# Kernel optimization log

Hardware: AMD Instinct MI355X
Metric: run time of the kernel (lower is better)

Reference implementation:

```python
import jax, jax.numpy as jnp
import numpy as np

B, N, E, FIN, D, A = 64, 512, 2048, 300, 256, 64
NH = 4
EPS = 1e-5


def setup_inputs() -> dict:
    ks = jax.random.split(jax.random.key(0), 32)
    lengths = 256 + jax.random.randint(ks[0], (B,), 0, N - 256 + 1)
    L = lengths[:, None]
    r = jax.random.randint(ks[1], (B, E), 0, 1 << 30)
    c = jax.random.randint(ks[2], (B, E), 0, 1 << 30)
    edge_row = r % L                                   # src in [0, len)
    edge_col = (edge_row + 1 + c % (L - 1)) % L        # dst != src, in [0, len)
    w = lambda k, sh, fan: jax.random.normal(k, sh, jnp.float32) / np.float32(np.sqrt(fan))
    b = lambda k, sh: 0.01 * jax.random.normal(k, sh, jnp.float32)
    return dict(
        x=jax.random.normal(ks[3], (B, N, FIN), jnp.float32),
        edge_attr=jax.random.normal(ks[4], (B, E, A), jnp.float32),
        edge_row=edge_row, edge_col=edge_col, lengths=lengths,
        W1=w(ks[5], (D, FIN), FIN), W2=w(ks[6], (D, A), A),
        W3=w(ks[7], (D, 2 * D), 2 * D), b3=b(ks[8], (D,)), gcn_bias=b(ks[9], (D,)),
        bn1_g=jnp.ones((D,)), bn1_b=jnp.zeros((D,)),
        in_proj_w=w(ks[10], (3 * D, D), D), in_proj_b=b(ks[11], (3 * D,)),
        out_proj_w=w(ks[12], (D, D), D), out_proj_b=b(ks[13], (D,)),
        ln1_g=jnp.ones((D,)), ln1_b=jnp.zeros((D,)),
        lin1_w=w(ks[14], (4 * D, D), D), lin1_b=b(ks[15], (4 * D,)),
        lin2_w=w(ks[16], (D, 4 * D), 4 * D), lin2_b=b(ks[17], (D,)),
        ln2_g=jnp.ones((D,)), ln2_b=jnp.zeros((D,)),
        bn2_g=jnp.ones((D,)), bn2_b=jnp.zeros((D,)),
        lin_w=w(ks[18], (2, 2 * D), 2 * D), lin_b=b(ks[19], (2,)),
        bn3_g=jnp.ones((2,)), bn3_b=jnp.zeros((2,)),
    )


def _bn(x, g, bt, axes):
    m = jnp.mean(x, axes, keepdims=True)
    v = jnp.mean((x - m) ** 2, axes, keepdims=True)
    return (x - m) / jnp.sqrt(v + EPS) * g + bt


def _ln(x, g, bt):
    m = jnp.mean(x, -1, keepdims=True)
    v = jnp.mean((x - m) ** 2, -1, keepdims=True)
    return (x - m) / jnp.sqrt(v + EPS) * g + bt


def _forward(x, edge_attr, edge_row, edge_col, lengths,
             W1, W2, W3, b3, gcn_bias, bn1_g, bn1_b,
             in_proj_w, in_proj_b, out_proj_w, out_proj_b, ln1_g, ln1_b,
             lin1_w, lin1_b, lin2_w, lin2_b, ln2_g, ln2_b, bn2_g, bn2_b,
             lin_w, lin_b, bn3_g, bn3_b):
    BN_ = B * N
    off = (jnp.arange(B, dtype=edge_row.dtype) * N)[:, None]
    row = (edge_row + off).reshape(-1)
    col = (edge_col + off).reshape(-1)
    sl = jnp.arange(BN_, dtype=row.dtype)            # one self-loop per node
    row_all = jnp.concatenate([row, sl])
    col_all = jnp.concatenate([col, sl])
    xs = x.reshape(BN_, FIN) @ W1.T                  # [BN, D]
    ea = edge_attr.reshape(B * E, A) @ W2.T          # [BE, D]
    ea_all = jnp.concatenate([ea, jnp.ones((BN_, D), xs.dtype)], 0)
    deg = jax.ops.segment_sum(jnp.ones_like(col_all, dtype=xs.dtype), col_all, BN_)
    dinv = deg ** -0.5                               # deg >= 1 (self loops)
    norm = dinv[row_all] * dinv[col_all]
    msg = norm[:, None] * (jnp.concatenate([xs[row_all], ea_all], -1) @ W3.T + b3)
    agg = jax.ops.segment_sum(msg, col_all, BN_) / deg[:, None]   # aggr='mean'
    h = jnp.tanh(agg + gcn_bias).reshape(B, N, D)
    mask = jnp.arange(N)[None, :] < lengths[:, None]              # pad_sequence zeros
    h = h * mask[..., None]
    h = _bn(h, bn1_g, bn1_b, (0, 1))
    # TransformerEncoderLayer (post-norm, relu, no dropout, no attn mask)
    qkv = h @ in_proj_w.T + in_proj_b
    q, k, v = jnp.split(qkv, 3, -1)
    dh = D // NH
    q = q.reshape(B, N, NH, dh); k = k.reshape(B, N, NH, dh); v = v.reshape(B, N, NH, dh)
    sc = jnp.einsum('bqhd,bkhd->bhqk', q, k) / np.float32(np.sqrt(dh))
    attn = jnp.einsum('bhqk,bkhd->bqhd', jax.nn.softmax(sc, -1), v).reshape(B, N, D)
    attn = attn @ out_proj_w.T + out_proj_b
    h1 = _ln(h + attn, ln1_g, ln1_b)
    ff = jax.nn.relu(h1 @ lin1_w.T + lin1_b) @ lin2_w.T + lin2_b
    h2 = _ln(h1 + ff, ln2_g, ln2_b)
    enc = _bn(h2, bn2_g, bn2_b, (0, 1))
    lenf = lengths.astype(enc.dtype)
    avg = jnp.sum(enc, 1) / lenf[:, None]            # sum over full padded length
    mx = jnp.max(jnp.where(mask[..., None], enc, -jnp.inf), 1)  # ragged max
    pool = jnp.concatenate([mx, avg], 1)
    res = _bn(pool @ lin_w.T + lin_b, bn3_g, bn3_b, (0,))
    return jax.nn.softmax(res, 1)


def reference(x, edge_attr, edge_row, edge_col, lengths,
              W1, W2, W3, b3, gcn_bias, bn1_g, bn1_b,
              in_proj_w, in_proj_b, out_proj_w, out_proj_b, ln1_g, ln1_b,
              lin1_w, lin1_b, lin2_w, lin2_b, ln2_g, ln2_b, bn2_g, bn2_b,
              lin_w, lin_b, bn3_g, bn3_b):
    return _forward(x, edge_attr, edge_row, edge_col, lengths,
                    W1, W2, W3, b3, gcn_bias, bn1_g, bn1_b,
                    in_proj_w, in_proj_b, out_proj_w, out_proj_b, ln1_g, ln1_b,
                    lin1_w, lin1_b, lin2_w, lin2_b, ln2_g, ln2_b, bn2_g, bn2_b,
                    lin_w, lin_b, bn3_g, bn3_b)
```

## Files before the change

kernel.cpp:

```cpp
#include <hip/hip_runtime.h>
#include <hip/hip_bf16.h>

#define BB   64
#define NN   512
#define EE   2048
#define FINK 300
#define DD   256
#define BN_TOT (BB*NN)
#define BE_TOT (BB*EE)
#define EPSF 1e-5f

using bf16 = __hip_bfloat16;
typedef unsigned short u16;
typedef __attribute__((ext_vector_type(8))) short short8;
typedef __attribute__((ext_vector_type(4))) float f32x4;
typedef __attribute__((ext_vector_type(4))) unsigned short u16x4;

__device__ __forceinline__ float tf(float x) { return x; }
__device__ __forceinline__ float tf(bf16 x)  { return __bfloat162float(x); }
__device__ __forceinline__ void  stv(float* p, float v) { *p = v; }
__device__ __forceinline__ void  stv(bf16*  p, float v) { *p = __float2bfloat16(v); }

__device__ __forceinline__ u16 f2bu(float f) {
    bf16 b = __float2bfloat16(f);
    return *(u16*)&b;
}
__device__ __forceinline__ void st4b(u16* p, f32x4 v)
{
    u16x4 o;
    o[0] = f2bu(v[0]); o[1] = f2bu(v[1]); o[2] = f2bu(v[2]); o[3] = f2bu(v[3]);
    *(u16x4*)p = o;
}

__device__ __forceinline__ void gload16(const void* g, void* l)
{
    __builtin_amdgcn_global_load_lds((const __attribute__((address_space(1))) void*)g,
                                     (__attribute__((address_space(3))) void*)l, 16, 0, 0);
}

__global__ void detect_kernel(const int* __restrict__ lengths, int* __restrict__ flags)
{
    flags[1] = (lengths[1] == 0) ? 1 : 0;
}

__global__ void conv_i(const void* __restrict__ src, int* __restrict__ dst, int n,
                       const int* __restrict__ flags)
{
    int i = blockIdx.x * 256 + threadIdx.x;
    if (i >= n) return;
    const int* s = (const int*)src;
    dst[i] = s[flags[1] ? (i << 1) : i];
}

__global__ void conv_i2(const void* __restrict__ src1, int* __restrict__ dst1,
                        const void* __restrict__ src2, int* __restrict__ dst2,
                        int n, const int* __restrict__ flags)
{
    int i = blockIdx.x * 256 + threadIdx.x;
    int wide = flags[1];
    if (i < n) {
        dst1[i] = ((const int*)src1)[wide ? (i << 1) : i];
    } else if (i < 2 * n) {
        int k = i - n;
        dst2[k] = ((const int*)src2)[wide ? (k << 1) : k];
    }
}

__global__ void conv_pad(const float* __restrict__ src, u16* __restrict__ dst, int rows,
                         int sk, int dk)
{
    int dk4 = dk >> 2;
    int i = blockIdx.x * 256 + threadIdx.x;
    if (i >= rows * dk4) return;
    int r = i / dk4, c4 = (i - r * dk4) * 4;
    if (c4 < sk) {
        f32x4 v = *(const f32x4*)&src[(size_t)r * sk + c4];
        st4b(&dst[(size_t)r * dk + c4], v);
    } else {
        *(u16x4*)&dst[(size_t)r * dk + c4] = (u16x4){0, 0, 0, 0};
    }
}

__global__ void conv_w4(const float* __restrict__ s0, u16* __restrict__ d0,
                        const float* __restrict__ s1, u16* __restrict__ d1,
                        const float* __restrict__ s2, u16* __restrict__ d2,
                        const float* __restrict__ s3, u16* __restrict__ d3)
{
    int i = blockIdx.x * 256 + threadIdx.x;
    const float* s; u16* d; int off;
    if (i < 49152)       { s = s0; d = d0; off = i; }
    else if (i < 65536)  { s = s1; d = d1; off = i - 49152; }
    else if (i < 131072) { s = s2; d = d2; off = i - 65536; }
    else                 { s = s3; d = d3; off = i - 131072; }
    f32x4 v = *(const f32x4*)&s[(size_t)off * 4];
    st4b(&d[(size_t)off * 4], v);
}

__global__ void prep_W13(const float* __restrict__ W3, const float* __restrict__ W1,
                         u16* __restrict__ W13b)
{
    int d = blockIdx.x;
    int f = threadIdx.x;
    float s = 0.f;
    if (f < FINK) {
        for (int j = 0; j < 256; j++)
            s += W3[d * 512 + j] * W1[j * FINK + f];
    }
    W13b[d * 320 + f] = f2bu(s);
}

template<typename TC, int RELU>
__global__ __launch_bounds__(256)
void gemm_bf(const u16* __restrict__ A, const u16* __restrict__ W,
             const float* __restrict__ bias, TC* __restrict__ C,
             int M, int N, int K, int lda, int ldw)
{
    __shared__ u16 As[128 * 32];
    __shared__ u16 Ws[128 * 32];

    const int m0 = blockIdx.y * 128;
    const int n0 = blockIdx.x * 128;
    const int tid  = threadIdx.x;
    const int lane = tid & 63;
    const int wv   = tid >> 6;
    const int fr   = lane & 15;
    const int q8   = (lane >> 4) * 8;
    const int mb   = (wv >> 1) * 64;
    const int nb   = (wv & 1) * 64;

    const int r16 = lane >> 2;
    const int c8  = (lane & 3) * 8;

    f32x4 acc[4][4];
#pragma unroll
    for (int i = 0; i < 4; i++)
#pragma unroll
        for (int j = 0; j < 4; j++) acc[i][j] = (f32x4){0.f, 0.f, 0.f, 0.f};

    for (int k0 = 0; k0 < K; k0 += 32) {
        __syncthreads();
#pragma unroll
        for (int j = 0; j < 2; j++) {
            int rowA = m0 + wv * 32 + j * 16 + r16;
            int rowW = n0 + wv * 32 + j * 16 + r16;
            gload16(A + (size_t)rowA * lda + k0 + c8, &As[(wv * 32 + j * 16) * 32]);
            gload16(W + (size_t)rowW * ldw + k0 + c8, &Ws[(wv * 32 + j * 16) * 32]);
        }
        __syncthreads();

        short8 af[4], bf[4];
#pragma unroll
        for (int i = 0; i < 4; i++) af[i] = *(const short8*)&As[(mb + i * 16 + fr) * 32 + q8];
#pragma unroll
        for (int j = 0; j < 4; j++) bf[j] = *(const short8*)&Ws[(nb + j * 16 + fr) * 32 + q8];
#pragma unroll
        for (int i = 0; i < 4; i++)
#pragma unroll
            for (int j = 0; j < 4; j++)
                acc[i][j] = __builtin_amdgcn_mfma_f32_16x16x32_bf16(af[i], bf[j], acc[i][j], 0, 0, 0);
    }

#pragma unroll
    for (int i = 0; i < 4; i++) {
#pragma unroll
        for (int j = 0; j < 4; j++) {
            int gn = n0 + nb + j * 16 + fr;
            float bv = bias ? bias[gn] : 0.f;
#pragma unroll
            for (int r = 0; r < 4; r++) {
                int gm = m0 + mb + i * 16 + (lane >> 4) * 4 + r;
                float v = acc[i][j][r] + bv;
                if (RELU) v = fmaxf(v, 0.f);
                stv(&C[(size_t)gm * N + gn], v);
            }
        }
    }
}

__global__ void prep_M(const float* __restrict__ W3, const float* __restrict__ W2,
                       u16* __restrict__ Mb, float* __restrict__ sb)
{
    int d = blockIdx.x, a = threadIdx.x;
    float s = 0.f;
    for (int j = 0; j < 256; j++)
        s += W3[d * 512 + 256 + j] * W2[j * 64 + a];
    Mb[d * 64 + a] = f2bu(s);
    if (a == 0) {
        float t = 0.f;
        for (int j = 0; j < 256; j++) t += W3[d * 512 + 256 + j];
        sb[d] = t;
    }
}

__global__ __launch_bounds__(512)
void sort_edges(const int* __restrict__ ecol, const int* __restrict__ erow,
                float* __restrict__ deg, int* __restrict__ node_off,
                uint2* __restrict__ edat)
{
    const int b = blockIdx.x;
    const int t = threadIdx.x;
    const int base = b * EE;
    __shared__ int cnt[512];
    __shared__ int tmp[512];
    __shared__ int off2[512];

    cnt[t] = 0;
    __syncthreads();
    for (int e = t; e < EE; e += 512) atomicAdd(&cnt[ecol[base + e]], 1);
    __syncthreads();

    int v = cnt[t];
    deg[b * NN + t] = (float)(v + 1);
    tmp[t] = v;
    __syncthreads();
    for (int s = 1; s < 512; s <<= 1) {
        int y = (t >= s) ? tmp[t - s] : 0;
        __syncthreads();
        tmp[t] += y;
        __syncthreads();
    }
    int excl = tmp[t] - v;
    node_off[b * NN + t] = excl;
    off2[t] = excl;
    __syncthreads();
    for (int e = t; e < EE; e += 512) {
        int c = ecol[base + e];
        int r = erow[base + e];
        int pos = atomicAdd(&off2[c], 1);
        float nrm = rsqrtf((float)((cnt[r] + 1) * (cnt[c] + 1)));
        edat[base + pos] = make_uint2(((unsigned)e << 16) | (unsigned)r,
                                      __float_as_uint(nrm));
    }
}

__global__ __launch_bounds__(256)
void edge_gather(const uint2* __restrict__ edat, const int* __restrict__ node_off,
                 const float* __restrict__ y1, const float* __restrict__ eattr,
                 float* __restrict__ agg1, u16* __restrict__ eaggb)
{
    const int j = blockIdx.x;
    const int b = j >> 9;
    const int cc = j & 511;
    const int tid  = threadIdx.x;
    const int wv   = tid >> 6;
    const int lane = tid & 63;
    const int start = node_off[j];
    const int end   = (cc == 511) ? EE : node_off[j + 1];

    f32x4 acc = (f32x4){0.f, 0.f, 0.f, 0.f};
    float acce = 0.f;
    for (int i = start + wv; i < end; i += 4) {
        uint2 ed = edat[(size_t)b * EE + i];
        float nw = __uint_as_float(ed.y);
        int r = (int)(ed.x & 0xffffu);
        int e = (int)(ed.x >> 16);
        f32x4 yv = *(const f32x4*)&y1[((size_t)(b * NN + r)) * 256 + lane * 4];
        acc += nw * yv;
        acce += nw * eattr[((size_t)(b * EE + e)) * 64 + lane];
    }

    __shared__ f32x4 redA[4][64];
    __shared__ float redB[4][64];
    redA[wv][lane] = acc;
    redB[wv][lane] = acce;
    __syncthreads();
    if (tid < 64) {
        f32x4 s = redA[0][tid];
        float se = redB[0][tid];
#pragma unroll
        for (int w = 1; w < 4; w++) { s += redA[w][tid]; se += redB[w][tid]; }
        *(f32x4*)&agg1[(size_t)j * 256 + tid * 4] = s;
        eaggb[(size_t)j * 64 + tid] = f2bu(se);
    }
}

__global__ void gcn_finalize(const float* __restrict__ agg1, float* __restrict__ aggM,
                             const float* __restrict__ y1, const float* __restrict__ sb,
                             const float* __restrict__ deg, const float* __restrict__ gcn_bias,
                             const int* __restrict__ lengths)
{
    int idx4 = blockIdx.x * 256 + threadIdx.x;
    int j  = idx4 >> 6;
    int d4 = (idx4 & 63) * 4;
    size_t base = (size_t)j * 256 + d4;
    float dg = deg[j];
    float inv = 1.f / dg;
    f32x4 a1 = *(const f32x4*)&agg1[base];
    f32x4 aM = *(const f32x4*)&aggM[base];
    f32x4 yv = *(const f32x4*)&y1[base];
    f32x4 sv = *(const f32x4*)&sb[d4];
    f32x4 gb = *(const f32x4*)&gcn_bias[d4];
    int b = j >> 9, p = j & 511;
    bool live = (p < lengths[b]);
    f32x4 o;
#pragma unroll
    for (int k = 0; k < 4; k++) {
        float a = (a1[k] + aM[k] + (yv[k] + sv[k]) * inv) * inv;
        o[k] = live ? tanhf(a + gb[k]) : 0.f;
    }
    *(f32x4*)&aggM[base] = o;
}

__global__ void bn_stats(const float* __restrict__ X, float* __restrict__ psum,
                         float* __restrict__ psumsq, int R)
{
    int wv = threadIdx.x >> 6, lane = threadIdx.x & 63;
    f32x4 s = (f32x4){0.f, 0.f, 0.f, 0.f};
    f32x4 q = (f32x4){0.f, 0.f, 0.f, 0.f};
    for (int r = blockIdx.x * 4 + wv; r < R; r += gridDim.x * 4) {
        f32x4 v = *(const f32x4*)&X[(size_t)r * DD + lane * 4];
        s += v; q += v * v;
    }
    __shared__ f32x4 rs[4][64], rq[4][64];
    rs[wv][lane] = s; rq[wv][lane] = q;
    __syncthreads();
    if (threadIdx.x < 64) {
        f32x4 ts = rs[0][lane], tq = rq[0][lane];
#pragma unroll
        for (int w = 1; w < 4; w++) { ts += rs[w][lane]; tq += rq[w][lane]; }
        *(f32x4*)&psum[blockIdx.x * DD + lane * 4]   = ts;
        *(f32x4*)&psumsq[blockIdx.x * DD + lane * 4] = tq;
    }
}

__global__ void bn_reduce(const float* __restrict__ psum, const float* __restrict__ psumsq,
                          float* __restrict__ sums, float* __restrict__ sumsq)
{
    int arr = blockIdx.x & 1;
    int chunk = blockIdx.x >> 1;
    int d = threadIdx.x;
    const float* src = arr ? psumsq : psum;
    float acc = 0.f;
    int i0 = chunk * 32;
    for (int i = i0; i < i0 + 32; i++) acc += src[i * DD + d];
    atomicAdd(arr ? &sumsq[d] : &sums[d], acc);
}

__global__ void bn_apply(float* __restrict__ X, const float* __restrict__ sums,
                         const float* __restrict__ sumsq, const float* __restrict__ g,
                         const float* __restrict__ bt, int R, u16* __restrict__ dup)
{
    int idx4 = blockIdx.x * 256 + threadIdx.x;
    int d4 = (idx4 & 63) * 4;
    size_t base = (size_t)idx4 * 4;
    float invR = 1.f / (float)R;
    f32x4 sm = *(const f32x4*)&sums[d4];
    f32x4 sq = *(const f32x4*)&sumsq[d4];
    f32x4 gv = *(const f32x4*)&g[d4];
    f32x4 bv = *(const f32x4*)&bt[d4];
    f32x4 x  = *(const f32x4*)&X[base];
    f32x4 o;
#pragma unroll
    for (int k = 0; k < 4; k++) {
        float m   = sm[k] * invR;
        float var = sq[k] * invR - m * m;
        o[k] = (x[k] - m) * rsqrtf(fmaxf(var, 0.f) + EPSF) * gv[k] + bv[k];
    }
    *(f32x4*)&X[base] = o;
    if (dup) st4b(&dup[base], o);
}

__global__ __launch_bounds__(512, 2)
void attn_mfma(const bf16* __restrict__ qkv, u16* __restrict__ out)
{
    const int bid = blockIdx.x;
    const int qp = bid >> 8;
    const int pr = bid & 255;
    const int h  = pr & 3;
    const int b  = pr >> 2;

    const int tid  = threadIdx.x;
    const int lane = tid & 63;
    const int wv   = tid >> 6;
    const int fr   = lane & 15;
    const int quad = lane >> 4;
    const int q8   = quad * 8;

    __shared__ u16 Ks[128][72];
    __shared__ u16 Vts[64][136];
    __shared__ u16 Ps[128][68];

    const u16* qb = (const u16*)qkv;
    const size_t bb = (size_t)(b * NN);
    const float CE = 0.125f * 1.44269504f;

    short8 aq[2];
#pragma unroll
    for (int ks = 0; ks < 2; ks++)
        aq[ks] = *(const short8*)(qb + (bb + qp * 128 + wv * 16 + fr) * 768
                                  + h * 64 + ks * 32 + q8);

    f32x4 O[4];
    float m_i[4], l_i[4];
#pragma unroll
    for (int t = 0; t < 4; t++) {
        O[t] = (f32x4){0.f, 0.f, 0.f, 0.f};
        m_i[t] = -1e30f; l_i[t] = 0.f;
    }

    for (int c = 0; c < 4; c++) {
        __syncthreads();
#pragma unroll
        for (int i = 0; i < 2; i++) {
            int idx = i * 512 + tid;
            int r = idx >> 3, seg = idx & 7;
            uint4 u = *((const uint4*)(qb + (bb + c * 128 + r) * 768 + 256 + h * 64) + seg);
            *(uint4*)&Ks[r][seg * 8] = u;
            uint4 v = *((const uint4*)(qb + (bb + c * 128 + r) * 768 + 512 + h * 64) + seg);
            u16* dst = &Vts[seg * 8][r ^ (seg << 3)];
            dst[0*136] = (u16)(v.x & 0xffff); dst[1*136] = (u16)(v.x >> 16);
            dst[2*136] = (u16)(v.y & 0xffff); dst[3*136] = (u16)(v.y >> 16);
            dst[4*136] = (u16)(v.z & 0xffff); dst[5*136] = (u16)(v.z >> 16);
            dst[6*136] = (u16)(v.w & 0xffff); dst[7*136] = (u16)(v.w >> 16);
        }
        __syncthreads();

        f32x4 S[8];
#pragma unroll
        for (int t = 0; t < 8; t++) S[t] = (f32x4){0.f, 0.f, 0.f, 0.f};
        __builtin_amdgcn_s_setprio(1);
#pragma unroll
        for (int ks = 0; ks < 2; ks++) {
#pragma unroll
            for (int t = 0; t < 8; t++) {
                short8 bk = *(const short8*)&Ks[t * 16 + fr][ks * 32 + q8];
                S[t] = __builtin_amdgcn_mfma_f32_16x16x32_bf16(aq[ks], bk, S[t], 0, 0, 0);
            }
        }
        __builtin_amdgcn_s_setprio(0);

        float mc[4];
#pragma unroll
        for (int r = 0; r < 4; r++) {
            float mm = -1e30f;
#pragma unroll
            for (int t = 0; t < 8; t++) mm = fmaxf(mm, S[t][r]);
            mc[r] = mm;
        }
#pragma unroll
        for (int msk = 1; msk < 16; msk <<= 1)
#pragma unroll
            for (int r = 0; r < 4; r++) mc[r] = fmaxf(mc[r], __shfl_xor(mc[r], msk));

        float alpha[4], ls[4];
#pragma unroll
        for (int r = 0; r < 4; r++) {
            float mn = fmaxf(m_i[r], mc[r]);
            alpha[r] = __builtin_amdgcn_exp2f((m_i[r] - mn) * CE);
            m_i[r] = mn;
            ls[r] = 0.f;
        }
#pragma unroll
        for (int t = 0; t < 4; t++)
#pragma unroll
            for (int r = 0; r < 4; r++) O[t][r] *= alpha[r];

#pragma unroll
        for (int hf = 0; hf < 2; hf++) {
#pragma unroll
            for (int tl = 0; tl < 4; tl++) {
                int t = hf * 4 + tl;
#pragma unroll
                for (int r = 0; r < 4; r++) {
                    float p = __builtin_amdgcn_exp2f((S[t][r] - m_i[r]) * CE);
                    Ps[wv * 16 + quad * 4 + r][tl * 16 + fr] = f2bu(p);
                    ls[r] += p;
                }
            }
            __builtin_amdgcn_s_setprio(1);
#pragma unroll
            for (int ks = 0; ks < 2; ks++) {
                short8 ap = *(const short8*)&Ps[wv * 16 + fr][ks * 32 + q8];
                int g = hf * 2 + ks;
#pragma unroll
                for (int t = 0; t < 4; t++) {
                    short8 bv = *(const short8*)&Vts[t * 16 + fr]
                                    [(g * 32 + q8) ^ ((t * 2 + (fr >> 3)) << 3)];
                    O[t] = __builtin_amdgcn_mfma_f32_16x16x32_bf16(ap, bv, O[t], 0, 0, 0);
                }
            }
            __builtin_amdgcn_s_setprio(0);
        }

#pragma unroll
        for (int msk = 1; msk < 16; msk <<= 1)
#pragma unroll
            for (int r = 0; r < 4; r++) ls[r] += __shfl_xor(ls[r], msk);
#pragma unroll
        for (int r = 0; r < 4; r++) l_i[r] = l_i[r] * alpha[r] + ls[r];
    }

#pragma unroll
    for (int t = 0; t < 4; t++)
#pragma unroll
        for (int r = 0; r < 4; r++) {
            int q = qp * 128 + wv * 16 + quad * 4 + r;
            out[(bb + q) * 256 + h * 64 + t * 16 + fr] = f2bu(O[t][r] / l_i[r]);
        }
}

__global__ void add_ln_kernel(const float* __restrict__ X, const float* __restrict__ Y,
                              const float* __restrict__ g, const float* __restrict__ bt,
                              float* __restrict__ out, u16* __restrict__ dup)
{
    int wv = threadIdx.x >> 6, lane = threadIdx.x & 63;
    int row = blockIdx.x * 4 + wv;
    size_t base = (size_t)row * DD + lane * 4;
    f32x4 v = *(const f32x4*)&X[base] + *(const f32x4*)&Y[base];
    float s = v[0] + v[1] + v[2] + v[3];
#pragma unroll
    for (int m = 1; m < 64; m <<= 1) s += __shfl_xor(s, m);
    float mean = s * (1.f / DD);
    f32x4 d;
#pragma unroll
    for (int k = 0; k < 4; k++) d[k] = v[k] - mean;
    float q = d[0]*d[0] + d[1]*d[1] + d[2]*d[2] + d[3]*d[3];
#pragma unroll
    for (int m = 1; m < 64; m <<= 1) q += __shfl_xor(q, m);
    float inv = rsqrtf(q * (1.f / DD) + EPSF);
    f32x4 gv = *(const f32x4*)&g[lane * 4];
    f32x4 bv = *(const f32x4*)&bt[lane * 4];
    f32x4 o;
#pragma unroll
    for (int k = 0; k < 4; k++) o[k] = d[k] * inv * gv[k] + bv[k];
    *(f32x4*)&out[base] = o;
    if (dup) st4b(&dup[base], o);
}

__global__ void pool_kernel(const float* __restrict__ enc, const int* __restrict__ lengths,
                            float* __restrict__ poolbuf)
{
    int b = blockIdx.x;
    int wv = threadIdx.x >> 6, lane = threadIdx.x & 63;
    int L = lengths[b];
    if (L < 1) L = 1;
    f32x4 s  = (f32x4){0.f, 0.f, 0.f, 0.f};
    f32x4 mx = (f32x4){-1e30f, -1e30f, -1e30f, -1e30f};
    for (int n = wv; n < NN; n += 4) {
        f32x4 v = *(const f32x4*)&enc[((size_t)b * NN + n) * DD + lane * 4];
        s += v;
        if (n < L) {
#pragma unroll
            for (int k = 0; k < 4; k++) mx[k] = fmaxf(mx[k], v[k]);
        }
    }
    __shared__ f32x4 rs[4][64], rm[4][64];
    rs[wv][lane] = s; rm[wv][lane] = mx;
    __syncthreads();
    if (threadIdx.x < 64) {
        f32x4 ts = rs[0][lane], tm = rm[0][lane];
#pragma unroll
        for (int w = 1; w < 4; w++) {
            ts += rs[w][lane];
#pragma unroll
            for (int k = 0; k < 4; k++) tm[k] = fmaxf(tm[k], rm[w][lane][k]);
        }
        float invL = 1.f / (float)L;
#pragma unroll
        for (int k = 0; k < 4; k++) {
            poolbuf[b * 512 + lane * 4 + k]       = tm[k];
            poolbuf[b * 512 + 256 + lane * 4 + k] = ts[k] * invL;
        }
    }
}

__global__ void head_kernel(const float* __restrict__ poolbuf, const float* __restrict__ lin_w,
                            const float* __restrict__ lin_b, const float* __restrict__ g,
                            const float* __restrict__ bt, float* __restrict__ out)
{
    int b = threadIdx.x;
    float r0 = lin_b[0], r1 = lin_b[1];
    for (int k = 0; k < 512; k++) {
        float p = poolbuf[b * 512 + k];
        r0 += p * lin_w[k];
        r1 += p * lin_w[512 + k];
    }
    __shared__ float s0[64], s1[64], mstat[4];
    s0[b] = r0; s1[b] = r1; __syncthreads();
    if (b == 0) {
        float a0 = 0, a1 = 0, q0 = 0, q1 = 0;
        for (int i = 0; i < 64; i++) { a0 += s0[i]; a1 += s1[i]; }
        a0 *= (1.f / 64.f); a1 *= (1.f / 64.f);
        for (int i = 0; i < 64; i++) {
            float d0 = s0[i] - a0, d1 = s1[i] - a1;
            q0 += d0 * d0; q1 += d1 * d1;
        }
        mstat[0] = a0; mstat[1] = a1; mstat[2] = q0 * (1.f / 64.f); mstat[3] = q1 * (1.f / 64.f);
    }
    __syncthreads();
    float z0 = (r0 - mstat[0]) * rsqrtf(mstat[2] + EPSF) * g[0] + bt[0];
    float z1 = (r1 - mstat[1]) * rsqrtf(mstat[3] + EPSF) * g[1] + bt[1];
    float mx = fmaxf(z0, z1);
    float e0 = __expf(z0 - mx), e1 = __expf(z1 - mx);
    float inv = 1.f / (e0 + e1);
    out[b * 2 + 0] = e0 * inv;
    out[b * 2 + 1] = e1 * inv;
}

extern "C" void kernel_launch(void* const* d_in, const int* in_sizes, int n_in,
                              void* d_out, int out_size, void* d_ws, size_t ws_size,
                              hipStream_t stream)
{
    (void)in_sizes; (void)n_in; (void)out_size; (void)ws_size;
    const float* x          = (const float*)d_in[0];
    const float* edge_attr  = (const float*)d_in[1];
    const float* W1         = (const float*)d_in[5];
    const float* W2         = (const float*)d_in[6];
    const float* W3         = (const float*)d_in[7];
    const float* b3         = (const float*)d_in[8];
    const float* gcn_bias   = (const float*)d_in[9];
    const float* bn1_g      = (const float*)d_in[10];
    const float* bn1_b      = (const float*)d_in[11];
    const float* in_proj_w  = (const float*)d_in[12];
    const float* in_proj_b  = (const float*)d_in[13];
    const float* out_proj_w = (const float*)d_in[14];
    const float* out_proj_b = (const float*)d_in[15];
    const float* ln1_g      = (const float*)d_in[16];
    const float* ln1_b      = (const float*)d_in[17];
    const float* lin1_w     = (const float*)d_in[18];
    const float* lin1_b     = (const float*)d_in[19];
    const float* lin2_w     = (const float*)d_in[20];
    const float* lin2_b     = (const float*)d_in[21];
    const float* ln2_g      = (const float*)d_in[22];
    const float* ln2_b      = (const float*)d_in[23];
    const float* bn2_g      = (const float*)d_in[24];
    const float* bn2_b      = (const float*)d_in[25];
    const float* lin_w      = (const float*)d_in[26];
    const float* lin_b      = (const float*)d_in[27];
    const float* bn3_g      = (const float*)d_in[28];
    const float* bn3_b      = (const float*)d_in[29];

    char* p = (char*)d_ws;
    u16*   big   = (u16*)p;   p += (size_t)BN_TOT * 1024 * 2;
    float* bufA  = (float*)p; p += (size_t)BN_TOT * 256 * 4;
    float* bufB  = (float*)p; p += (size_t)BN_TOT * 256 * 4;
    float* bufC  = (float*)p; p += (size_t)BN_TOT * 256 * 4;
    u16*   bufP  = (u16*)p;   p += (size_t)BN_TOT * 256 * 2;
    float* deg   = (float*)p; p += (size_t)BN_TOT * 4;
    u16*   Mb    = (u16*)p;   p += 256 * 64 * 2;
    float* sb    = (float*)p; p += 1024;
    float* stats = (float*)p; p += 4 * 256 * 4;
    float* psum  = (float*)p; p += 512 * 256 * 4;
    float* psumsq= (float*)p; p += 512 * 256 * 4;
    float* poolbuf=(float*)p; p += 64 * 512 * 4;
    int*   flags = (int*)p;   p += 256;
    int*   erc   = (int*)p;   p += BE_TOT * 4;
    int*   ecc   = (int*)p;   p += BE_TOT * 4;
    int*   lenc  = (int*)p;   p += 256;
    uint2* edat  = (uint2*)p; p += (size_t)BE_TOT * 8;
    int*   noff  = (int*)p;   p += BN_TOT * 4;
    u16*   W13b  = (u16*)p;   p += 256 * 320 * 2;
    u16*   ipwb  = (u16*)p;   p += 768 * 256 * 2;
    u16*   opwb  = (u16*)p;   p += 256 * 256 * 2;
    u16*   l1wb  = (u16*)p;   p += 1024 * 256 * 2;
    u16*   l2wb  = (u16*)p;   p += 256 * 1024 * 2;

    u16* xb    = big;
    u16* eaggb = big + (size_t)BN_TOT * (320+256);
    bf16* qkv  = (bf16*)big;
    bf16* ffa  = (bf16*)big;

    float* y1      = bufB;
    float* agg1    = bufC;
    float* aggM    = bufA;
    float* h       = bufA;
    u16*   hb      = bufP;
    u16*   attnoutb= bufP;
    float* attnp   = bufB;
    float* h1      = bufC;
    u16*   h1b     = bufP;
    float* ffb     = bufA;
    float* h2      = bufB;

    hipMemsetAsync(stats, 0, 4 * 256 * 4, stream);

    detect_kernel<<<1, 1, 0, stream>>>((const int*)d_in[4], flags);
    conv_i2<<<(2 * BE_TOT + 255) / 256, 256, 0, stream>>>(d_in[2], erc, d_in[3], ecc,
                                                          BE_TOT, flags);
    conv_i<<<1, 64, 0, stream>>>(d_in[4], lenc, BB, flags);

    conv_pad<<<(BN_TOT * 80 + 255) / 256, 256, 0, stream>>>(x, xb, BN_TOT, FINK, 320);
    conv_w4<<<768, 256, 0, stream>>>(in_proj_w, ipwb, out_proj_w, opwb,
                                     lin1_w, l1wb, lin2_w, l2wb);

    prep_W13<<<256, 320, 0, stream>>>(W3, W1, W13b);
    prep_M<<<256, 64, 0, stream>>>(W3, W2, Mb, sb);
    sort_edges<<<BB, 512, 0, stream>>>(ecc, erc, deg, noff, edat);

    gemm_bf<float, 0><<<dim3(2, 256), 256, 0, stream>>>(
        xb, W13b, b3, y1, BN_TOT, 256, 320, 320, 320);

    edge_gather<<<BN_TOT, 256, 0, stream>>>(edat, noff, y1, edge_attr, agg1, eaggb);
    gemm_bf<float, 0><<<dim3(2, 256), 256, 0, stream>>>(
        eaggb, Mb, nullptr, aggM, BN_TOT, 256, 64, 64, 64);

    gcn_finalize<<<BN_TOT / 4, 256, 0, stream>>>(agg1, aggM, y1, sb, deg, gcn_bias, lenc);

    bn_stats<<<512, 256, 0, stream>>>(h, psum, psumsq, BN_TOT);
    bn_reduce<<<32, 256, 0, stream>>>(psum, psumsq, stats, stats + 256);
    bn_apply<<<BN_TOT / 4, 256, 0, stream>>>(h, stats, stats + 256, bn1_g, bn1_b, BN_TOT, hb);

    gemm_bf<bf16, 0><<<dim3(6, 256), 256, 0, stream>>>(
        hb, ipwb, in_proj_b, qkv, BN_TOT, 768, 256, 256, 256);

    attn_mfma<<<BB * 4 * 4, 512, 0, stream>>>(qkv, attnoutb);

    gemm_bf<float, 0><<<dim3(2, 256), 256, 0, stream>>>(
        attnoutb, opwb, out_proj_b, attnp, BN_TOT, 256, 256, 256, 256);

    add_ln_kernel<<<BN_TOT / 4, 256, 0, stream>>>(h, attnp, ln1_g, ln1_b, h1, h1b);

    gemm_bf<bf16, 1><<<dim3(8, 256), 256, 0, stream>>>(
        h1b, l1wb, lin1_b, ffa, BN_TOT, 1024, 256, 256, 256);
    gemm_bf<float, 0><<<dim3(2, 256), 256, 0, stream>>>(
        (const u16*)ffa, l2wb, lin2_b, ffb, BN_TOT, 256, 1024, 1024, 1024);

    add_ln_kernel<<<BN_TOT / 4, 256, 0, stream>>>(h1, ffb, ln2_g, ln2_b, h2, nullptr);

    bn_stats<<<512, 256, 0, stream>>>(h2, psum, psumsq, BN_TOT);
    bn_reduce<<<32, 256, 0, stream>>>(psum, psumsq, stats + 512, stats + 768);
    bn_apply<<<BN_TOT / 4, 256, 0, stream>>>(h2, stats + 512, stats + 768, bn2_g, bn2_b, BN_TOT, nullptr);

    pool_kernel<<<64, 256, 0, stream>>>(h2, lenc, poolbuf);
    head_kernel<<<1, 64, 0, stream>>>(poolbuf, lin_w, lin_b, bn3_g, bn3_b, (float*)d_out);
}
```

Before: 593.5 us.

## Double GEMM K-tile with XOR-swizzled LDS and fuse final batchnorm into pooling

The bf16 MFMA GEMM now stages 64-wide K slices instead of 32. It uses an XOR swizzle on the LDS column index so fragment reads avoid bank conflicts, which halves the number of barrier pairs per K. Separately, the standalone bn_apply pass over h2 is removed. The normalisation is applied on the fly inside the pooling kernel from the precomputed sums, which saves a full read and write of the activation tensor. The risks are higher LDS use per block, and that the variance now comes from sumsq/R minus mean squared, which depends on the stats layout matching what pool_norm expects.

```diff
diff --git a/kernel.cpp b/kernel.cpp
--- a/kernel.cpp
+++ b/kernel.cpp
@@ -115,8 +115,8 @@
              const float* __restrict__ bias, TC* __restrict__ C,
              int M, int N, int K, int lda, int ldw)
 {
-    __shared__ u16 As[128 * 32];
-    __shared__ u16 Ws[128 * 32];
+    __shared__ u16 As[128 * 64];
+    __shared__ u16 Ws[128 * 64];
 
     const int m0 = blockIdx.y * 128;
     const int n0 = blockIdx.x * 128;
@@ -128,8 +128,9 @@
     const int mb   = (wv >> 1) * 64;
     const int nb   = (wv & 1) * 64;
 
-    const int r16 = lane >> 2;
-    const int c8  = (lane & 3) * 8;
+    const int r8  = lane >> 3;
+    const int csw = 8 * ((lane & 7) ^ r8);
+    const int frx = (fr & 7) << 3;
 
     f32x4 acc[4][4];
 #pragma unroll
@@ -137,27 +138,31 @@
 #pragma unroll
         for (int j = 0; j < 4; j++) acc[i][j] = (f32x4){0.f, 0.f, 0.f, 0.f};
 
-    for (int k0 = 0; k0 < K; k0 += 32) {
+    for (int k0 = 0; k0 < K; k0 += 64) {
         __syncthreads();
 #pragma unroll
-        for (int j = 0; j < 2; j++) {
-            int rowA = m0 + wv * 32 + j * 16 + r16;
-            int rowW = n0 + wv * 32 + j * 16 + r16;
-            gload16(A + (size_t)rowA * lda + k0 + c8, &As[(wv * 32 + j * 16) * 32]);
-            gload16(W + (size_t)rowW * ldw + k0 + c8, &Ws[(wv * 32 + j * 16) * 32]);
+        for (int j = 0; j < 4; j++) {
+            int rowA = m0 + wv * 32 + j * 8 + r8;
+            int rowW = n0 + wv * 32 + j * 8 + r8;
+            gload16(A + (size_t)rowA * lda + k0 + csw, &As[(wv * 32 + j * 8) * 64]);
+            gload16(W + (size_t)rowW * ldw + k0 + csw, &Ws[(wv * 32 + j * 8) * 64]);
         }
         __syncthreads();
 
-        short8 af[4], bf[4];
-#pragma unroll
-        for (int i = 0; i < 4; i++) af[i] = *(const short8*)&As[(mb + i * 16 + fr) * 32 + q8];
-#pragma unroll
-        for (int j = 0; j < 4; j++) bf[j] = *(const short8*)&Ws[(nb + j * 16 + fr) * 32 + q8];
-#pragma unroll
-        for (int i = 0; i < 4; i++)
-#pragma unroll
-            for (int j = 0; j < 4; j++)
-                acc[i][j] = __builtin_amdgcn_mfma_f32_16x16x32_bf16(af[i], bf[j], acc[i][j], 0, 0, 0);
+#pragma unroll
+        for (int ks = 0; ks < 2; ks++) {
+            int rc = (ks * 32 + q8) ^ frx;
+            short8 af[4], bf[4];
+#pragma unroll
+            for (int i = 0; i < 4; i++) af[i] = *(const short8*)&As[(mb + i * 16 + fr) * 64 + rc];
+#pragma unroll
+            for (int j = 0; j < 4; j++) bf[j] = *(const short8*)&Ws[(nb + j * 16 + fr) * 64 + rc];
+#pragma unroll
+            for (int i = 0; i < 4; i++)
+#pragma unroll
+                for (int j = 0; j < 4; j++)
+                    acc[i][j] = __builtin_amdgcn_mfma_f32_16x16x32_bf16(af[i], bf[j], acc[i][j], 0, 0, 0);
+        }
     }
 
 #pragma unroll
@@ -527,17 +532,33 @@
     if (dup) st4b(&dup[base], o);
 }
 
-__global__ void pool_kernel(const float* __restrict__ enc, const int* __restrict__ lengths,
-                            float* __restrict__ poolbuf)
+__global__ void pool_norm(const float* __restrict__ enc, const int* __restrict__ lengths,
+                          const float* __restrict__ sums, const float* __restrict__ sumsq,
+                          const float* __restrict__ g, const float* __restrict__ bt,
+                          int R, float* __restrict__ poolbuf)
 {
     int b = blockIdx.x;
     int wv = threadIdx.x >> 6, lane = threadIdx.x & 63;
     int L = lengths[b];
     if (L < 1) L = 1;
+    float invR = 1.f / (float)R;
+    f32x4 sm = *(const f32x4*)&sums[lane * 4];
+    f32x4 sq = *(const f32x4*)&sumsq[lane * 4];
+    f32x4 gv = *(const f32x4*)&g[lane * 4];
+    f32x4 bv = *(const f32x4*)&bt[lane * 4];
+    f32x4 mean, rsv;
+#pragma unroll
+    for (int k = 0; k < 4; k++) {
+        mean[k] = sm[k] * invR;
+        float var = sq[k] * invR - mean[k] * mean[k];
+        rsv[k] = rsqrtf(fmaxf(var, 0.f) + EPSF) * gv[k];
+    }
     f32x4 s  = (f32x4){0.f, 0.f, 0.f, 0.f};
     f32x4 mx = (f32x4){-1e30f, -1e30f, -1e30f, -1e30f};
     for (int n = wv; n < NN; n += 4) {
         f32x4 v = *(const f32x4*)&enc[((size_t)b * NN + n) * DD + lane * 4];
+#pragma unroll
+        for (int k = 0; k < 4; k++) v[k] = (v[k] - mean[k]) * rsv[k] + bv[k];
         s += v;
         if (n < L) {
 #pragma unroll
@@ -719,8 +740,8 @@
 
     bn_stats<<<512, 256, 0, stream>>>(h2, psum, psumsq, BN_TOT);
     bn_reduce<<<32, 256, 0, stream>>>(psum, psumsq, stats + 512, stats + 768);
-    bn_apply<<<BN_TOT / 4, 256, 0, stream>>>(h2, stats + 512, stats + 768, bn2_g, bn2_b, BN_TOT, nullptr);
-
-    pool_kernel<<<64, 256, 0, stream>>>(h2, lenc, poolbuf);
+
+    pool_norm<<<64, 256, 0, stream>>>(h2, lenc, stats + 512, stats + 768,
+                                      bn2_g, bn2_b, BN_TOT, poolbuf);
     head_kernel<<<1, 64, 0, stream>>>(poolbuf, lin_w, lin_b, bn3_g, bn3_b, (float*)d_out);
 }
```

After: 575.1 us. 3.1% less time.
